# Performance work log

Measured on AMD Instinct MI355X. Metric: run time of the kernel, lower is better.

The kernel has to match this reference:

```python
import jax, jax.numpy as jnp
import numpy as np

FEATURE_DIM = 256
KEEP = 64  # low-frequency block size kept after the pseudo-DCT


def setup_inputs() -> dict:
    key = jax.random.key(0)
    k_x, k_w, k_b = jax.random.split(key, 3)
    B, C, H, W = 32, 3, 512, 512
    x = jax.random.uniform(k_x, (B, C, H, W), dtype=jnp.float32)
    # nn.Linear(64*64, feature_dim): weight [out, in], bias [out]
    fan_in = KEEP * KEEP
    bound = 1.0 / np.sqrt(fan_in)
    fc_w = jax.random.uniform(k_w, (FEATURE_DIM, fan_in), dtype=jnp.float32, minval=-bound, maxval=bound)
    fc_b = jax.random.uniform(k_b, (FEATURE_DIM,), dtype=jnp.float32, minval=-bound, maxval=bound)
    return {"x": x, "fc_w": fc_w, "fc_b": fc_b}


def reference(x, fc_w, fc_b):
    # grayscale conversion (input has 3 channels)
    x_gray = 0.299 * x[:, 0] + 0.587 * x[:, 1] + 0.114 * x[:, 2]  # [B, H, W]
    # "dct2d": FFT along last dim, then FFT along second-to-last, real part
    X = jnp.fft.fft(jnp.fft.fft(x_gray, axis=-1), axis=-2).real  # [B, H, W]
    # keep low-frequency 64x64 block and flatten
    coeffs = X[:, :KEEP, :KEEP].reshape(x.shape[0], KEEP * KEEP)  # [B, 4096]
    # final linear projection
    return coeffs @ fc_w.T + fc_b  # [B, feature_dim]
```

## Files before the change

### kernel.cpp

```cpp
#include <hip/hip_runtime.h>
#include <hip/hip_bf16.h>

#define HW_ (512 * 512)

typedef __attribute__((ext_vector_type(8))) _Float16 half8;
typedef __attribute__((ext_vector_type(4))) _Float16 half4;
typedef __attribute__((ext_vector_type(4))) float    f32x4;

__global__ __launch_bounds__(256) void k_prep(_Float16* __restrict__ basisA) {
    int i = blockIdx.x * 256 + threadIdx.x;
    if (i < 128 * 512) {
        int r = i >> 9, h = i & 511;
        int ph = ((r & 63) * h) & 511;
        float ang = (float)ph * (6.28318530717958647692f / 512.0f);
        basisA[i] = (_Float16)((r < 64) ? cosf(ang) : sinf(ang));
    }
}

__global__ __launch_bounds__(256) void k1(const float* __restrict__ x,
                                          const _Float16* __restrict__ basisA,
                                          _Float16* __restrict__ P)
{
    __shared__ _Float16 g[32][520];
    int h0 = blockIdx.x * 32;
    int b  = blockIdx.y;
    int t  = threadIdx.x;
    const float* xb = x + (size_t)b * 3 * HW_;

    for (int i = 0; i < 16; ++i) {
        int slot = t + i * 256;
        int hh = slot >> 7;
        int w4 = slot & 127;
        const float* p = xb + (size_t)(h0 + hh) * 512 + w4 * 4;
        float4 r  = *(const float4*)p;
        float4 gg = *(const float4*)(p + HW_);
        float4 bb = *(const float4*)(p + 2 * HW_);
        half4 o;
        o.x = (_Float16)(0.299f * r.x + 0.587f * gg.x + 0.114f * bb.x);
        o.y = (_Float16)(0.299f * r.y + 0.587f * gg.y + 0.114f * bb.y);
        o.z = (_Float16)(0.299f * r.z + 0.587f * gg.z + 0.114f * bb.z);
        o.w = (_Float16)(0.299f * r.w + 0.587f * gg.w + 0.114f * bb.w);
        *(half4*)&g[hh][w4 * 4] = o;
    }
    __syncthreads();

    int lane = t & 63, wv = t >> 6, l15 = lane & 15, quad = lane >> 4;
    f32x4 acc[2][2];
    for (int i = 0; i < 2; ++i)
        for (int j = 0; j < 2; ++j) acc[i][j] = (f32x4){0.f, 0.f, 0.f, 0.f};

    for (int k0 = 0; k0 < 512; k0 += 32) {
        int kc = k0 + quad * 8;
        half8 a[2], bv[2];
        for (int mi = 0; mi < 2; ++mi)
            a[mi] = *(const half8*)(basisA + (wv * 32 + mi * 16 + l15) * 512 + kc);
        for (int ni = 0; ni < 2; ++ni)
            bv[ni] = *(const half8*)&g[ni * 16 + l15][kc];
        for (int mi = 0; mi < 2; ++mi)
            for (int ni = 0; ni < 2; ++ni)
                acc[mi][ni] = __builtin_amdgcn_mfma_f32_16x16x32_f16(
                    a[mi], bv[ni], acc[mi][ni], 0, 0, 0);
    }

    _Float16* Pb = P + (size_t)b * 128 * 512;
    for (int mi = 0; mi < 2; ++mi)
        for (int ni = 0; ni < 2; ++ni)
            for (int r = 0; r < 4; ++r) {
                int m = wv * 32 + mi * 16 + quad * 4 + r;
                int h = h0 + ni * 16 + l15;
                float v = acc[mi][ni][r];
                if (m >= 64) v = -v;
                Pb[m * 512 + h] = (_Float16)v;
            }
}

__global__ __launch_bounds__(128) void k2(const _Float16* __restrict__ basisA,
                                          const _Float16* __restrict__ P,
                                          _Float16* __restrict__ X)
{
    int b     = blockIdx.y;
    int mbase = blockIdx.x * 32 + (threadIdx.x >> 6) * 16;
    int lane  = threadIdx.x & 63, l15 = lane & 15, quad = lane >> 4;

    f32x4 acc[4];
    for (int i = 0; i < 4; ++i) acc[i] = (f32x4){0.f, 0.f, 0.f, 0.f};

    const _Float16* Pb = P + (size_t)b * 128 * 512;

    for (int k0 = 0; k0 < 1024; k0 += 32) {
        int kc  = k0 + quad * 8;
        int hi  = (kc >= 512) ? 64 : 0;
        int col = kc & 511;
        half8 a = *(const half8*)(basisA + (hi + mbase + l15) * 512 + col);
        for (int ni = 0; ni < 4; ++ni) {
            half8 bv = *(const half8*)(Pb + (hi + ni * 16 + l15) * 512 + col);
            acc[ni] = __builtin_amdgcn_mfma_f32_16x16x32_f16(a, bv, acc[ni], 0, 0, 0);
        }
    }

    _Float16* Xb = X + (size_t)b * 4096;
    for (int ni = 0; ni < 4; ++ni)
        for (int r = 0; r < 4; ++r) {
            int kh = mbase + quad * 4 + r;
            int kw = ni * 16 + l15;
            Xb[kh * 64 + kw] = (_Float16)(acc[ni][r] * 0.0625f);
        }
}

__global__ __launch_bounds__(64) void k3(const _Float16* __restrict__ X,
                                         const float* __restrict__ fc_w,
                                         const float* __restrict__ fc_b,
                                         float* __restrict__ out)
{
    int nb  = blockIdx.x & 15;
    int kcb = blockIdx.x >> 4;
    int lane = threadIdx.x, l15 = lane & 15, quad = lane >> 4;

    f32x4 acc[2];
    acc[0] = (f32x4){0.f, 0.f, 0.f, 0.f};
    acc[1] = (f32x4){0.f, 0.f, 0.f, 0.f};

    int kbeg = kcb * 1024;
    for (int k0 = kbeg; k0 < kbeg + 1024; k0 += 32) {
        int kk = k0 + quad * 8;
        half8 a0 = *(const half8*)(X + (size_t)l15 * 4096 + kk);
        half8 a1 = *(const half8*)(X + (size_t)(16 + l15) * 4096 + kk);
        const float* wp = fc_w + (size_t)(nb * 16 + l15) * 4096 + kk;
        float4 f0 = *(const float4*)wp;
        float4 f1 = *(const float4*)(wp + 4);
        half8 b0;
        b0[0] = (_Float16)(f0.x * 16.0f);
        b0[1] = (_Float16)(f0.y * 16.0f);
        b0[2] = (_Float16)(f0.z * 16.0f);
        b0[3] = (_Float16)(f0.w * 16.0f);
        b0[4] = (_Float16)(f1.x * 16.0f);
        b0[5] = (_Float16)(f1.y * 16.0f);
        b0[6] = (_Float16)(f1.z * 16.0f);
        b0[7] = (_Float16)(f1.w * 16.0f);
        acc[0] = __builtin_amdgcn_mfma_f32_16x16x32_f16(a0, b0, acc[0], 0, 0, 0);
        acc[1] = __builtin_amdgcn_mfma_f32_16x16x32_f16(a1, b0, acc[1], 0, 0, 0);
    }

    for (int mi = 0; mi < 2; ++mi)
        for (int r = 0; r < 4; ++r) {
            int m = mi * 16 + quad * 4 + r;
            int f = nb * 16 + l15;
            float v = acc[mi][r];
            if (kcb == 0) v += fc_b[f];
            atomicAdd(out + m * 256 + f, v);
        }
}

extern "C" void kernel_launch(void* const* d_in, const int* in_sizes, int n_in,
                              void* d_out, int out_size, void* d_ws, size_t ws_size,
                              hipStream_t stream) {
    const float* x    = (const float*)d_in[0];
    const float* fc_w = (const float*)d_in[1];
    const float* fc_b = (const float*)d_in[2];
    float* out = (float*)d_out;

    char* ws = (char*)d_ws;
    _Float16* basisA = (_Float16*)(ws + 0);
    _Float16* P      = (_Float16*)(ws + 131072);
    _Float16* X      = (_Float16*)(ws + 4325376);

    k_prep<<<256, 256, 0, stream>>>(basisA);
    k1<<<dim3(16, 32), 256, 0, stream>>>(x, basisA, P);
    k2<<<dim3(2, 32), 128, 0, stream>>>(basisA, P, X);
    hipMemsetAsync(d_out, 0, (size_t)out_size * sizeof(float), stream);
    k3<<<64, 64, 0, stream>>>(X, fc_w, fc_b, out);
}
```

Before: 189.1 us.

## Pre-swizzle operands into MFMA fragment layout and split-K with LDS reduction

Stores the DFT bases, the intermediate P, the coefficients X and a pre-converted fp16 copy of fc_w in MFMA-fragment-ordered layouts, so each lane does one contiguous half8 load per fragment instead of strided row loads. k1 halves its row tile to launch twice as many blocks. k2 and k3 split K across waves and reduce through shared memory, which removes the memset and the atomicAdd epilogue. The cost is extra prep work converting fc_w on every call, plus more complex index arithmetic that could hide layout bugs.

Result: faster. 178.4 us (-5.7%).

```diff
diff --git a/kernel.cpp b/kernel.cpp
--- a/kernel.cpp
+++ b/kernel.cpp
@@ -1,5 +1,4 @@
 #include <hip/hip_runtime.h>
-#include <hip/hip_bf16.h>
 
 #define HW_ (512 * 512)
 
@@ -7,30 +6,64 @@
 typedef __attribute__((ext_vector_type(4))) _Float16 half4;
 typedef __attribute__((ext_vector_type(4))) float    f32x4;
 
-__global__ __launch_bounds__(256) void k_prep(_Float16* __restrict__ basisA) {
-    int i = blockIdx.x * 256 + threadIdx.x;
-    if (i < 128 * 512) {
-        int r = i >> 9, h = i & 511;
-        int ph = ((r & 63) * h) & 511;
+__global__ __launch_bounds__(256) void k_prep(const float* __restrict__ fc_w,
+                                              _Float16* __restrict__ bF1,
+                                              _Float16* __restrict__ bF2,
+                                              _Float16* __restrict__ whF)
+{
+    int id = blockIdx.x * 256 + threadIdx.x;
+    if (id < 65536) {
+        int j = id & 7, lane = (id >> 3) & 63;
+        int mt = (id >> 9) & 7, ks = id >> 12;
+        int m = mt * 16 + (lane & 15);
+        int k = ks * 32 + ((lane >> 4) << 3) + j;
+        int ph = ((m & 63) * k) & 511;
         float ang = (float)ph * (6.28318530717958647692f / 512.0f);
-        basisA[i] = (_Float16)((r < 64) ? cosf(ang) : sinf(ang));
+        bF1[id] = (_Float16)((m < 64) ? cosf(ang) : sinf(ang));
+    } else if (id < 131072) {
+        int id2 = id - 65536;
+        int j = id2 & 7, lane = (id2 >> 3) & 63;
+        int kt = (id2 >> 9) & 3, t = id2 >> 11;
+        int kh = kt * 16 + (lane & 15);
+        int kg = t * 32 + ((lane >> 4) << 3) + j;
+        int h = kg & 511;
+        int ph = (kh * h) & 511;
+        float ang = (float)ph * (6.28318530717958647692f / 512.0f);
+        bF2[id2] = (_Float16)((kg < 512) ? cosf(ang) : sinf(ang));
+    } else {
+        int idx8 = id - 131072;
+        int lane = idx8 & 63;
+        int f = ((idx8 >> 6) & 15) * 16 + (lane & 15);
+        int k = (idx8 >> 10) * 32 + ((lane >> 4) << 3);
+        const float* wp = fc_w + (size_t)f * 4096 + k;
+        float4 f0 = *(const float4*)wp;
+        float4 f1 = *(const float4*)(wp + 4);
+        half8 o;
+        o[0] = (_Float16)(f0.x * 16.0f);
+        o[1] = (_Float16)(f0.y * 16.0f);
+        o[2] = (_Float16)(f0.z * 16.0f);
+        o[3] = (_Float16)(f0.w * 16.0f);
+        o[4] = (_Float16)(f1.x * 16.0f);
+        o[5] = (_Float16)(f1.y * 16.0f);
+        o[6] = (_Float16)(f1.z * 16.0f);
+        o[7] = (_Float16)(f1.w * 16.0f);
+        *(half8*)(whF + (size_t)idx8 * 8) = o;
     }
 }
 
 __global__ __launch_bounds__(256) void k1(const float* __restrict__ x,
-                                          const _Float16* __restrict__ basisA,
-                                          _Float16* __restrict__ P)
-{
-    __shared__ _Float16 g[32][520];
-    int h0 = blockIdx.x * 32;
+                                          const _Float16* __restrict__ bF1,
+                                          _Float16* __restrict__ PF)
+{
+    __shared__ _Float16 g[16][520];
+    int h0 = blockIdx.x * 16;
     int b  = blockIdx.y;
     int t  = threadIdx.x;
     const float* xb = x + (size_t)b * 3 * HW_;
 
-    for (int i = 0; i < 16; ++i) {
+    for (int i = 0; i < 8; ++i) {
         int slot = t + i * 256;
-        int hh = slot >> 7;
-        int w4 = slot & 127;
+        int hh = slot >> 7, w4 = slot & 127;
         const float* p = xb + (size_t)(h0 + hh) * 512 + w4 * 4;
         float4 r  = *(const float4*)p;
         float4 gg = *(const float4*)(p + HW_);
@@ -45,110 +78,108 @@
     __syncthreads();
 
     int lane = t & 63, wv = t >> 6, l15 = lane & 15, quad = lane >> 4;
-    f32x4 acc[2][2];
-    for (int i = 0; i < 2; ++i)
-        for (int j = 0; j < 2; ++j) acc[i][j] = (f32x4){0.f, 0.f, 0.f, 0.f};
-
-    for (int k0 = 0; k0 < 512; k0 += 32) {
-        int kc = k0 + quad * 8;
-        half8 a[2], bv[2];
-        for (int mi = 0; mi < 2; ++mi)
-            a[mi] = *(const half8*)(basisA + (wv * 32 + mi * 16 + l15) * 512 + kc);
-        for (int ni = 0; ni < 2; ++ni)
-            bv[ni] = *(const half8*)&g[ni * 16 + l15][kc];
-        for (int mi = 0; mi < 2; ++mi)
-            for (int ni = 0; ni < 2; ++ni)
-                acc[mi][ni] = __builtin_amdgcn_mfma_f32_16x16x32_f16(
-                    a[mi], bv[ni], acc[mi][ni], 0, 0, 0);
-    }
-
-    _Float16* Pb = P + (size_t)b * 128 * 512;
-    for (int mi = 0; mi < 2; ++mi)
-        for (int ni = 0; ni < 2; ++ni)
-            for (int r = 0; r < 4; ++r) {
-                int m = wv * 32 + mi * 16 + quad * 4 + r;
-                int h = h0 + ni * 16 + l15;
-                float v = acc[mi][ni][r];
-                if (m >= 64) v = -v;
-                Pb[m * 512 + h] = (_Float16)v;
-            }
-}
-
-__global__ __launch_bounds__(128) void k2(const _Float16* __restrict__ basisA,
-                                          const _Float16* __restrict__ P,
-                                          _Float16* __restrict__ X)
-{
-    int b     = blockIdx.y;
-    int mbase = blockIdx.x * 32 + (threadIdx.x >> 6) * 16;
-    int lane  = threadIdx.x & 63, l15 = lane & 15, quad = lane >> 4;
-
-    f32x4 acc[4];
-    for (int i = 0; i < 4; ++i) acc[i] = (f32x4){0.f, 0.f, 0.f, 0.f};
-
-    const _Float16* Pb = P + (size_t)b * 128 * 512;
-
-    for (int k0 = 0; k0 < 1024; k0 += 32) {
-        int kc  = k0 + quad * 8;
-        int hi  = (kc >= 512) ? 64 : 0;
-        int col = kc & 511;
-        half8 a = *(const half8*)(basisA + (hi + mbase + l15) * 512 + col);
-        for (int ni = 0; ni < 4; ++ni) {
-            half8 bv = *(const half8*)(Pb + (hi + ni * 16 + l15) * 512 + col);
-            acc[ni] = __builtin_amdgcn_mfma_f32_16x16x32_f16(a, bv, acc[ni], 0, 0, 0);
-        }
-    }
-
-    _Float16* Xb = X + (size_t)b * 4096;
-    for (int ni = 0; ni < 4; ++ni)
-        for (int r = 0; r < 4; ++r) {
-            int kh = mbase + quad * 4 + r;
-            int kw = ni * 16 + l15;
-            Xb[kh * 64 + kw] = (_Float16)(acc[ni][r] * 0.0625f);
-        }
-}
-
-__global__ __launch_bounds__(64) void k3(const _Float16* __restrict__ X,
-                                         const float* __restrict__ fc_w,
-                                         const float* __restrict__ fc_b,
-                                         float* __restrict__ out)
-{
-    int nb  = blockIdx.x & 15;
-    int kcb = blockIdx.x >> 4;
-    int lane = threadIdx.x, l15 = lane & 15, quad = lane >> 4;
-
     f32x4 acc[2];
     acc[0] = (f32x4){0.f, 0.f, 0.f, 0.f};
     acc[1] = (f32x4){0.f, 0.f, 0.f, 0.f};
 
-    int kbeg = kcb * 1024;
-    for (int k0 = kbeg; k0 < kbeg + 1024; k0 += 32) {
-        int kk = k0 + quad * 8;
-        half8 a0 = *(const half8*)(X + (size_t)l15 * 4096 + kk);
-        half8 a1 = *(const half8*)(X + (size_t)(16 + l15) * 4096 + kk);
-        const float* wp = fc_w + (size_t)(nb * 16 + l15) * 4096 + kk;
-        float4 f0 = *(const float4*)wp;
-        float4 f1 = *(const float4*)(wp + 4);
-        half8 b0;
-        b0[0] = (_Float16)(f0.x * 16.0f);
-        b0[1] = (_Float16)(f0.y * 16.0f);
-        b0[2] = (_Float16)(f0.z * 16.0f);
-        b0[3] = (_Float16)(f0.w * 16.0f);
-        b0[4] = (_Float16)(f1.x * 16.0f);
-        b0[5] = (_Float16)(f1.y * 16.0f);
-        b0[6] = (_Float16)(f1.z * 16.0f);
-        b0[7] = (_Float16)(f1.w * 16.0f);
-        acc[0] = __builtin_amdgcn_mfma_f32_16x16x32_f16(a0, b0, acc[0], 0, 0, 0);
-        acc[1] = __builtin_amdgcn_mfma_f32_16x16x32_f16(a1, b0, acc[1], 0, 0, 0);
-    }
-
+    for (int k0 = 0; k0 < 512; k0 += 32) {
+        half8 bv = *(const half8*)&g[l15][k0 + quad * 8];
+        for (int mi = 0; mi < 2; ++mi) {
+            half8 a = *(const half8*)(bF1 +
+                (size_t)(((k0 >> 5) * 8 + wv * 2 + mi) * 64 + lane) * 8);
+            acc[mi] = __builtin_amdgcn_mfma_f32_16x16x32_f16(a, bv, acc[mi], 0, 0, 0);
+        }
+    }
+
+    _Float16* Pb = PF + (size_t)b * 65536;
+    int h = h0 + l15;
     for (int mi = 0; mi < 2; ++mi)
         for (int r = 0; r < 4; ++r) {
-            int m = mi * 16 + quad * 4 + r;
-            int f = nb * 16 + l15;
+            int m = wv * 32 + mi * 16 + quad * 4 + r;
             float v = acc[mi][r];
-            if (kcb == 0) v += fc_b[f];
-            atomicAdd(out + m * 256 + f, v);
+            int m64 = m & 63;
+            int tt  = (m < 64) ? (h >> 5) : 16 + (h >> 5);
+            if (m >= 64) v = -v;
+            int lp = (m64 & 15) | (((h >> 3) & 3) << 4);
+            Pb[(size_t)((tt * 4 + (m64 >> 4)) * 64 + lp) * 8 + (h & 7)] = (_Float16)v;
         }
+}
+
+__global__ __launch_bounds__(256) void k2(const _Float16* __restrict__ bF2,
+                                          const _Float16* __restrict__ PF,
+                                          _Float16* __restrict__ XF)
+{
+    __shared__ float red[2][64][17];
+    int b = blockIdx.y;
+    int lane = threadIdx.x & 63, wv = threadIdx.x >> 6;
+    int l15 = lane & 15, quad = lane >> 4;
+    int khtile = blockIdx.x * 2 + (wv & 1);
+    int khalf  = wv >> 1;
+
+    const _Float16* Pb = PF + (size_t)b * 65536;
+    f32x4 acc[4];
+    for (int i = 0; i < 4; ++i) acc[i] = (f32x4){0.f, 0.f, 0.f, 0.f};
+
+    int t0 = khalf * 16;
+    for (int tt = t0; tt < t0 + 16; ++tt) {
+        half8 a = *(const half8*)(bF2 + (size_t)((tt * 4 + khtile) * 64 + lane) * 8);
+        for (int ni = 0; ni < 4; ++ni) {
+            half8 bv = *(const half8*)(Pb + (size_t)((tt * 4 + ni) * 64 + lane) * 8);
+            acc[ni] = __builtin_amdgcn_mfma_f32_16x16x32_f16(a, bv, acc[ni], 0, 0, 0);
+        }
+    }
+
+    if (khalf)
+        for (int ni = 0; ni < 4; ++ni)
+            for (int r = 0; r < 4; ++r)
+                red[wv & 1][lane][ni * 4 + r] = acc[ni][r];
+    __syncthreads();
+    if (!khalf)
+        for (int ni = 0; ni < 4; ++ni)
+            for (int r = 0; r < 4; ++r) {
+                float v = acc[ni][r] + red[wv][lane][ni * 4 + r];
+                int kh = khtile * 16 + quad * 4 + r;
+                int kw = ni * 16 + l15;
+                int k  = kh * 64 + kw;
+                int lp = (b & 15) | (((k >> 3) & 3) << 4);
+                XF[(size_t)(((k >> 5) * 2 + (b >> 4)) * 64 + lp) * 8 + (k & 7)] =
+                    (_Float16)(v * 0.0625f);
+            }
+}
+
+__global__ __launch_bounds__(512) void k3(const _Float16* __restrict__ XF,
+                                          const _Float16* __restrict__ whF,
+                                          const float* __restrict__ fc_b,
+                                          float* __restrict__ out)
+{
+    __shared__ float red[8][64][9];
+    int nb = blockIdx.x;
+    int tid = threadIdx.x;
+    int lane = tid & 63, wv = tid >> 6;
+
+    f32x4 acc[2];
+    acc[0] = (f32x4){0.f, 0.f, 0.f, 0.f};
+    acc[1] = (f32x4){0.f, 0.f, 0.f, 0.f};
+
+    for (int it = 0; it < 16; ++it) {
+        int tt = wv * 16 + it;
+        half8 a0 = *(const half8*)(XF + (size_t)((tt * 2 + 0) * 64 + lane) * 8);
+        half8 a1 = *(const half8*)(XF + (size_t)((tt * 2 + 1) * 64 + lane) * 8);
+        half8 bv = *(const half8*)(whF + (size_t)((tt * 16 + nb) * 64 + lane) * 8);
+        acc[0] = __builtin_amdgcn_mfma_f32_16x16x32_f16(a0, bv, acc[0], 0, 0, 0);
+        acc[1] = __builtin_amdgcn_mfma_f32_16x16x32_f16(a1, bv, acc[1], 0, 0, 0);
+    }
+
+    for (int j = 0; j < 8; ++j)
+        red[wv][lane][j] = acc[j >> 2][j & 3];
+    __syncthreads();
+
+    int lp = tid >> 3, j = tid & 7;
+    float s = 0.f;
+    for (int w = 0; w < 8; ++w) s += red[w][lp][j];
+    int batch = (j >> 2) * 16 + (lp >> 4) * 4 + (j & 3);
+    int f = nb * 16 + (lp & 15);
+    out[batch * 256 + f] = s + fc_b[f];
 }
 
 extern "C" void kernel_launch(void* const* d_in, const int* in_sizes, int n_in,
@@ -160,13 +191,14 @@
     float* out = (float*)d_out;
 
     char* ws = (char*)d_ws;
-    _Float16* basisA = (_Float16*)(ws + 0);
-    _Float16* P      = (_Float16*)(ws + 131072);
-    _Float16* X      = (_Float16*)(ws + 4325376);
-
-    k_prep<<<256, 256, 0, stream>>>(basisA);
-    k1<<<dim3(16, 32), 256, 0, stream>>>(x, basisA, P);
-    k2<<<dim3(2, 32), 128, 0, stream>>>(basisA, P, X);
-    hipMemsetAsync(d_out, 0, (size_t)out_size * sizeof(float), stream);
-    k3<<<64, 64, 0, stream>>>(X, fc_w, fc_b, out);
-}
+    _Float16* bF1 = (_Float16*)(ws);
+    _Float16* bF2 = (_Float16*)(ws + 131072);
+    _Float16* whF = (_Float16*)(ws + 262144);
+    _Float16* PF  = (_Float16*)(ws + 2359296);
+    _Float16* XF  = (_Float16*)(ws + 6553600);
+
+    k_prep<<<1024, 256, 0, stream>>>(fc_w, bF1, bF2, whF);
+    k1<<<dim3(32, 32), 256, 0, stream>>>(x, bF1, PF);
+    k2<<<dim3(2, 32), 256, 0, stream>>>(bF2, PF, XF);
+    k3<<<16, 512, 0, stream>>>(XF, whF, fc_b, out);
+}
```
